# Kernel optimization log

Measured on AMD Instinct MI355X. Metric: run time of the kernel, lower is better.

## Reference

```python
import math
import jax, jax.numpy as jnp
import numpy as np

VOCAB_SHAPE = (50, 50, 80)   # prod = 200000
EMBED_SHAPE = (8, 4, 4)      # prod = 128
TT_RANK = 16
N_INDICES = 8192
VOCAB_SIZE = 200000


def _make_core(key, r_l, v, e, r_r):
    scale = 1.0 / math.sqrt(r_l * v * e * r_r + 1)
    return scale * jax.random.normal(key, (r_l, v, e, r_r), dtype=jnp.float32)


def setup_inputs() -> dict:
    key = jax.random.key(0)
    k0, k1, k2, ki = jax.random.split(key, 4)
    core0 = _make_core(k0, 1, VOCAB_SHAPE[0], EMBED_SHAPE[0], TT_RANK)
    core1 = _make_core(k1, TT_RANK, VOCAB_SHAPE[1], EMBED_SHAPE[1], TT_RANK)
    core2 = _make_core(k2, TT_RANK, VOCAB_SHAPE[2], EMBED_SHAPE[2], 1)
    indices = jax.random.randint(ki, (N_INDICES,), 0, VOCAB_SIZE, dtype=jnp.int64)
    return {"indices": indices, "core0": core0, "core1": core1, "core2": core2}


def _tt_to_dense(cores):
    # cores[k]: (r_l, v_k, e_k, r_r). Contract ranks left-to-right, keeping
    # vocab modes grouped before embed modes (row-major multi-index).
    W = cores[0][0]  # (v0, e0, r1)
    V, E = W.shape[0], W.shape[1]
    for G in cores[1:]:
        # (V, E, r) x (r, w, f, s) -> (V, w, E, f, s)
        W = jnp.einsum('ver,rwfs->vwefs', W, G)
        V *= G.shape[1]
        E *= G.shape[2]
        W = W.reshape(V, E, G.shape[3])
    return W.reshape(V, E)  # (vocab_size, embed_dim)


def reference(indices, core0, core1, core2):
    W = _tt_to_dense([core0, core1, core2])  # (vocab_size, embed_dim)
    return W[indices]  # (N, embed_dim)
```

## Files before the change

kernel.cpp:

```cpp
#include <hip/hip_runtime.h>


#define V1 50
#define V2 80
#define RR 16
#define NIDX 8192
#define NPAIR (V1 * V2)

__global__ __launch_bounds__(256) void tt_k1(
    const float* __restrict__ c1,
    const float* __restrict__ c2,
    float* __restrict__ w12)
{
    const int o = blockIdx.x * 256 + threadIdx.x;
    const int e1 = o & 3;
    const int r1 = (o >> 2) & 15;
    const int pair = o >> 6;
    const int i1 = pair / V2;
    const int i2 = pair - i1 * V2;

    const float4* B4 = (const float4*)(c1 + (((size_t)r1 * V1 + i1) * 4 + e1) * RR);
    float b[RR];
#pragma unroll
    for (int q = 0; q < 4; ++q) {
        float4 v = B4[q];
        b[q * 4 + 0] = v.x; b[q * 4 + 1] = v.y;
        b[q * 4 + 2] = v.z; b[q * 4 + 3] = v.w;
    }

    float o0 = 0.f, o1 = 0.f, o2 = 0.f, o3 = 0.f;
    const float4* C4 = (const float4*)(c2 + (size_t)i2 * 4);
#pragma unroll
    for (int r2 = 0; r2 < RR; ++r2) {
        float4 c = C4[(size_t)r2 * V2];
        o0 = fmaf(b[r2], c.x, o0);
        o1 = fmaf(b[r2], c.y, o1);
        o2 = fmaf(b[r2], c.z, o2);
        o3 = fmaf(b[r2], c.w, o3);
    }
    ((float4*)w12)[o] = make_float4(o0, o1, o2, o3);
}

__global__ __launch_bounds__(256) void tt_k2(
    const int* __restrict__ indices,
    const float* __restrict__ c0,
    const float* __restrict__ w12,
    float* __restrict__ out)
{
    const int t = blockIdx.x * 256 + threadIdx.x;
    const int n = t >> 5;
    const int sub = t & 31;
    const int e0 = sub >> 2;
    const int e1 = sub & 3;

    const int i  = indices[n];
    const int i0 = i / (V1 * V2);
    const int pair = i - i0 * (V1 * V2);

    const float4* A4 = (const float4*)(c0 + ((size_t)i0 * 8 + e0) * RR);
    float a[RR];
#pragma unroll
    for (int q = 0; q < 4; ++q) {
        float4 v = A4[q];
        a[q * 4 + 0] = v.x; a[q * 4 + 1] = v.y;
        a[q * 4 + 2] = v.z; a[q * 4 + 3] = v.w;
    }

    const float4* W4 = (const float4*)w12 + (size_t)pair * 64 + e1;
    float o0 = 0.f, o1 = 0.f, o2 = 0.f, o3 = 0.f;
#pragma unroll
    for (int r1 = 0; r1 < RR; ++r1) {
        float4 w = W4[(size_t)r1 * 4];
        o0 = fmaf(a[r1], w.x, o0);
        o1 = fmaf(a[r1], w.y, o1);
        o2 = fmaf(a[r1], w.z, o2);
        o3 = fmaf(a[r1], w.w, o3);
    }

    *(float4*)(out + (size_t)n * 128 + sub * 4) = make_float4(o0, o1, o2, o3);
}

extern "C" void kernel_launch(void* const* d_in, const int* in_sizes, int n_in,
                              void* d_out, int out_size, void* d_ws, size_t ws_size,
                              hipStream_t stream) {
    const int*   indices = (const int*)d_in[0];
    const float* c0      = (const float*)d_in[1];
    const float* c1      = (const float*)d_in[2];
    const float* c2      = (const float*)d_in[3];
    float*       out     = (float*)d_out;
    float*       w12     = (float*)d_ws;

    tt_k1<<<1000, 256, 0, stream>>>(c1, c2, w12);
    tt_k2<<<1024, 256, 0, stream>>>(indices, c0, w12, out);
}
```

Before: 15.69 us.

## Fuse TT core contraction into single per-index gather kernel using LDS

Replaces the two-kernel scheme, which first builds the full core1×core2 product table in workspace and then gathers from it, with one fused kernel. Each block takes 8 indices, computes the needed core1·core2 partial products for just those indices into shared memory, syncs, then contracts with core0 and writes the output. This drops a kernel launch and the global workspace round trip. In exchange it recomputes the partial product for duplicate pair indices, which is 8192 per-index products against the 4000 computed before.

```diff
diff --git a/kernel.cpp b/kernel.cpp
--- a/kernel.cpp
+++ b/kernel.cpp
@@ -5,57 +5,64 @@
 #define V2 80
 #define RR 16
 #define NIDX 8192
-#define NPAIR (V1 * V2)
+#define IDX_PER_BLOCK 8
 
-__global__ __launch_bounds__(256) void tt_k1(
+__global__ __launch_bounds__(256) void tt_fused(
+    const int* __restrict__ indices,
+    const float* __restrict__ c0,
     const float* __restrict__ c1,
     const float* __restrict__ c2,
-    float* __restrict__ w12)
+    float* __restrict__ out)
 {
-    const int o = blockIdx.x * 256 + threadIdx.x;
-    const int e1 = o & 3;
-    const int r1 = (o >> 2) & 15;
-    const int pair = o >> 6;
-    const int i1 = pair / V2;
-    const int i2 = pair - i1 * V2;
+    __shared__ float4 T[IDX_PER_BLOCK * 64];
 
-    const float4* B4 = (const float4*)(c1 + (((size_t)r1 * V1 + i1) * 4 + e1) * RR);
-    float b[RR];
+    const int t = threadIdx.x;
+    const int nbase = blockIdx.x * IDX_PER_BLOCK;
+
 #pragma unroll
-    for (int q = 0; q < 4; ++q) {
-        float4 v = B4[q];
-        b[q * 4 + 0] = v.x; b[q * 4 + 1] = v.y;
-        b[q * 4 + 2] = v.z; b[q * 4 + 3] = v.w;
+    for (int s = 0; s < 2; ++s) {
+        const int task = t + s * 256;
+        const int e1  = task & 3;
+        const int r1  = (task >> 2) & 15;
+        const int idx = task >> 6;
+
+        const int i    = indices[nbase + idx];
+        const int i0   = i / (V1 * V2);
+        const int pair = i - i0 * (V1 * V2);
+        const int i1   = pair / V2;
+        const int i2   = pair - i1 * V2;
+
+        const float4* B4 = (const float4*)(c1 + (((size_t)r1 * V1 + i1) * 4 + e1) * RR);
+        float b[RR];
+#pragma unroll
+        for (int q = 0; q < 4; ++q) {
+            float4 v = B4[q];
+            b[q * 4 + 0] = v.x; b[q * 4 + 1] = v.y;
+            b[q * 4 + 2] = v.z; b[q * 4 + 3] = v.w;
+        }
+
+        const float4* C4 = (const float4*)(c2 + (size_t)i2 * 4);
+        float o0 = 0.f, o1 = 0.f, o2 = 0.f, o3 = 0.f;
+#pragma unroll
+        for (int r2 = 0; r2 < RR; ++r2) {
+            float4 c = C4[(size_t)r2 * V2];
+            o0 = fmaf(b[r2], c.x, o0);
+            o1 = fmaf(b[r2], c.y, o1);
+            o2 = fmaf(b[r2], c.z, o2);
+            o3 = fmaf(b[r2], c.w, o3);
+        }
+        T[task] = make_float4(o0, o1, o2, o3);
     }
 
-    float o0 = 0.f, o1 = 0.f, o2 = 0.f, o3 = 0.f;
-    const float4* C4 = (const float4*)(c2 + (size_t)i2 * 4);
-#pragma unroll
-    for (int r2 = 0; r2 < RR; ++r2) {
-        float4 c = C4[(size_t)r2 * V2];
-        o0 = fmaf(b[r2], c.x, o0);
-        o1 = fmaf(b[r2], c.y, o1);
-        o2 = fmaf(b[r2], c.z, o2);
-        o3 = fmaf(b[r2], c.w, o3);
-    }
-    ((float4*)w12)[o] = make_float4(o0, o1, o2, o3);
-}
+    __syncthreads();
 
-__global__ __launch_bounds__(256) void tt_k2(
-    const int* __restrict__ indices,
-    const float* __restrict__ c0,
-    const float* __restrict__ w12,
-    float* __restrict__ out)
-{
-    const int t = blockIdx.x * 256 + threadIdx.x;
-    const int n = t >> 5;
-    const int sub = t & 31;
-    const int e0 = sub >> 2;
-    const int e1 = sub & 3;
+    const int e1  = t & 3;
+    const int e0  = (t >> 2) & 7;
+    const int idx = t >> 5;
+    const int n   = nbase + idx;
 
     const int i  = indices[n];
     const int i0 = i / (V1 * V2);
-    const int pair = i - i0 * (V1 * V2);
 
     const float4* A4 = (const float4*)(c0 + ((size_t)i0 * 8 + e0) * RR);
     float a[RR];
@@ -66,18 +73,18 @@
         a[q * 4 + 2] = v.z; a[q * 4 + 3] = v.w;
     }
 
-    const float4* W4 = (const float4*)w12 + (size_t)pair * 64 + e1;
+    const float4* Tb = &T[idx * 64 + e1];
     float o0 = 0.f, o1 = 0.f, o2 = 0.f, o3 = 0.f;
 #pragma unroll
     for (int r1 = 0; r1 < RR; ++r1) {
-        float4 w = W4[(size_t)r1 * 4];
+        float4 w = Tb[r1 * 4];
         o0 = fmaf(a[r1], w.x, o0);
         o1 = fmaf(a[r1], w.y, o1);
         o2 = fmaf(a[r1], w.z, o2);
         o3 = fmaf(a[r1], w.w, o3);
     }
 
-    *(float4*)(out + (size_t)n * 128 + sub * 4) = make_float4(o0, o1, o2, o3);
+    *(float4*)(out + (size_t)n * 128 + (e0 * 4 + e1) * 4) = make_float4(o0, o1, o2, o3);
 }
 
 extern "C" void kernel_launch(void* const* d_in, const int* in_sizes, int n_in,
@@ -88,8 +95,7 @@
     const float* c1      = (const float*)d_in[2];
     const float* c2      = (const float*)d_in[3];
     float*       out     = (float*)d_out;
-    float*       w12     = (float*)d_ws;
 
-    tt_k1<<<1000, 256, 0, stream>>>(c1, c2, w12);
-    tt_k2<<<1024, 256, 0, stream>>>(indices, c0, w12, out);
+    const int grid = NIDX / IDX_PER_BLOCK;
+    tt_fused<<<grid, 256, 0, stream>>>(indices, c0, c1, c2, out);
 }
```

Result: faster. 12.98 us (-17.2%).
